# Optimization experiments

Measured on AMD Instinct MI355X. Metric: run time of the kernel, lower is better.

The kernel has to match this reference:

```python
import jax, jax.numpy as jnp
import numpy as np

PROJ_DIM = 128
TEMP = 0.1
CLAMP_VAL = 50.0
EPS = 1e-6


def _coords(H, W):
    # [H*W, 2] grid of (x, y) coordinates, matching torch meshgrid indexing='ij'
    xs = jnp.arange(W, dtype=jnp.float32)
    ys = jnp.arange(H, dtype=jnp.float32)
    grid_y, grid_x = jnp.meshgrid(ys, xs, indexing='ij')
    return jnp.stack([grid_x.reshape(-1), grid_y.reshape(-1)], axis=-1)


def setup_inputs() -> dict:
    key = jax.random.key(0)
    k1, k2 = jax.random.split(key)
    B, C, H, W = 2, 128, 96, 96
    fL = jax.random.normal(k1, (B, C, H, W), dtype=jnp.float32)
    fR = jax.random.normal(k2, (B, C, H, W), dtype=jnp.float32)
    return {"fL": fL, "fR": fR}


def reference(fL, fR):
    B, C, H, W = fL.shape
    HW = H * W
    scale = jnp.float32(np.sqrt(PROJ_DIM))

    # L2-normalize over channel dim with epsilon clamp
    fLn = fL / jnp.maximum(jnp.linalg.norm(fL, axis=1, keepdims=True), EPS)
    fRn = fR / jnp.maximum(jnp.linalg.norm(fR, axis=1, keepdims=True), EPS)

    q = fLn.reshape(B, C, HW).transpose(0, 2, 1).astype(jnp.float32)  # [B, HW, C]
    k = fRn.reshape(B, C, HW).astype(jnp.float32)                      # [B, C, HW]

    coords = _coords(H, W)  # [HW, 2]

    # Global correlation: [B, HW, HW] (chunking in the original is math-equivalent)
    corr = jnp.einsum('bqc,bck->bqk', q, k) / scale
    corr = jnp.clip(corr / TEMP, -CLAMP_VAL, CLAMP_VAL)
    prob = jax.nn.softmax(corr, axis=-1)

    expected_pos = prob @ coords                 # [B, HW, 2]
    max_prob = jnp.max(prob, axis=-1)            # [B, HW]

    flow_abs = expected_pos.reshape(B, H, W, 2).transpose(0, 3, 1, 2)  # [B, 2, H, W]
    conf = max_prob.reshape(B, 1, H, W)

    src = coords.reshape(H, W, 2).transpose(2, 0, 1)[None]  # [1, 2, H, W]
    flow = (flow_abs - src).astype(fL.dtype)
    conf = conf.astype(fL.dtype)
    return flow, conf
```

## Files before the change

kernel.cpp:

```cpp
#include <hip/hip_runtime.h>
#include <stdint.h>

#define HW 9216
#define CDIM 128
#define WIDTH 96
#define BATCH 2

#define QSCALE 1.2753324954171245f

typedef _Float16 half8 __attribute__((ext_vector_type(8)));
typedef float float4v __attribute__((ext_vector_type(4)));
typedef float float2v __attribute__((ext_vector_type(2)));

__global__ __launch_bounds__(256) void norm_kernel(const float* __restrict__ fL,
                                                   const float* __restrict__ fR,
                                                   _Float16* __restrict__ Qh,
                                                   _Float16* __restrict__ Kh)
{
    __shared__ float ssred[4][64];
    __shared__ _Float16 ot[64 * 130];

    const float* src = (blockIdx.y == 0) ? fL : fR;
    _Float16* dst    = (blockIdx.y == 0) ? Qh : Kh;
    const float outScale = (blockIdx.y == 0) ? QSCALE : 1.0f;

    const int t = threadIdx.x;
    const int pos_l = t & 63, cg = t >> 6;
    const int pos0 = blockIdx.x * 64;
    const int b = pos0 / HW, pos_in = pos0 % HW + pos_l;

    const float* p = src + (size_t)b * CDIM * HW + pos_in;

    float v[32];
    float ss = 0.f;
    #pragma unroll
    for (int j = 0; j < 32; ++j) {
        v[j] = p[(size_t)(cg * 32 + j) * HW];
        ss += v[j] * v[j];
    }
    ssred[cg][pos_l] = ss;
    __syncthreads();
    float tot = ssred[0][pos_l] + ssred[1][pos_l] + ssred[2][pos_l] + ssred[3][pos_l];
    float scale = outScale / fmaxf(sqrtf(tot), 1e-6f);

    #pragma unroll
    for (int j = 0; j < 32; ++j)
        ot[pos_l * 130 + cg * 32 + j] = (_Float16)(v[j] * scale);
    __syncthreads();

    uint4* og = (uint4*)(dst + (size_t)(b * HW + pos0 % HW + 0) * CDIM);
    #pragma unroll
    for (int i = 0; i < 4; ++i) {
        int idx = i * 256 + t;
        int row = idx >> 4, chunk = idx & 15;
        og[idx] = *(const uint4*)&ot[row * 130 + chunk * 8];
    }
}

__global__ __launch_bounds__(256) void attn_kernel(const _Float16* __restrict__ Qh,
                                                   const _Float16* __restrict__ Kh,
                                                   float4* __restrict__ part)
{
    __shared__ _Float16 Ks[2 * 64 * 128];

    const int qt = blockIdx.x, split = blockIdx.y, b = blockIdx.z;
    const int t = threadIdx.x;
    const int lane = t & 63, wave = t >> 6;
    const int wq = wave >> 1, wk = wave & 1;
    const int lane15 = lane & 15, quad = lane >> 4;

    half8 af[2][4];
    {
        const char* qb = (const char*)(Qh +
            ((size_t)(b * HW + qt * 64 + wq * 32 + lane15)) * CDIM);
        #pragma unroll
        for (int mt = 0; mt < 2; ++mt)
            #pragma unroll
            for (int kc = 0; kc < 4; ++kc)
                af[mt][kc] = *(const half8*)(qb + mt * 16 * 256 + kc * 64 + quad * 16);
    }

    const int kbase0 = split * 1152;
    const char* kp0 = (const char*)(Kh + (size_t)b * HW * CDIM) + (size_t)kbase0 * 256;

    int voff[4];
    #pragma unroll
    for (int i = 0; i < 4; ++i) {
        int r = wave * 16 + i * 4 + quad;
        voff[i] = r * 256 + ((lane15 ^ (r & 15)) << 4);
    }

    #define STAGE(TILE, BUF)                                                     \
        {                                                                        \
            const char* kb_ = kp0 + (TILE) * 16384;                              \
            _Float16* db_ = &Ks[(BUF) * 8192 + wave * 16 * 128];                 \
            _Pragma("unroll")                                                    \
            for (int i_ = 0; i_ < 4; ++i_)                                       \
                __builtin_amdgcn_global_load_lds(                                \
                    (const __attribute__((address_space(1))) uint32_t*)(kb_ + voff[i_]), \
                    (__attribute__((address_space(3))) uint32_t*)(db_ + i_ * 4 * 128),   \
                    16, 0, 0);                                                   \
        }

    int rdoff[2][4];
    #pragma unroll
    for (int nt = 0; nt < 2; ++nt)
        #pragma unroll
        for (int kc = 0; kc < 4; ++kc)
            rdoff[nt][kc] = ((wk * 32 + nt * 16 + lane15) << 8) +
                            (((kc * 4 + quad) ^ lane15) << 4);
    const char* ksb = (const char*)&Ks[0];

    float xph[3][2], yph[3][2];
    {
        int off0 = wk * 32 + lane15;
        #pragma unroll
        for (int p = 0; p < 3; ++p) {
            #pragma unroll
            for (int nt = 0; nt < 2; ++nt) {
                int k = p * 64 + off0 + nt * 16;
                xph[p][nt] = (float)(k % 96);
                yph[p][nt] = (float)(split * 12 + k / 96);
            }
        }
    }

    float2v l2[4], ax2[4], ay2[4], mx2[4];
    #pragma unroll
    for (int p = 0; p < 4; ++p) {
        l2[p] = (float2v)0.f; ax2[p] = (float2v)0.f; ay2[p] = (float2v)0.f;
        mx2[p] = (float2v)(-1.0e30f);
    }

    STAGE(0, 0);
    __syncthreads();

    #pragma unroll
    for (int kt = 0; kt < 18; ++kt) {
        const int cur = kt & 1;
        const int phase = kt % 3;
        const float yadd = (float)(2 * (kt / 3));

        if (kt < 17) STAGE(kt + 1, 1 - cur);

        float4v acc[2][2];
        #pragma unroll
        for (int kc = 0; kc < 4; ++kc) {
            half8 bf[2];
            #pragma unroll
            for (int nt = 0; nt < 2; ++nt)
                bf[nt] = *(const half8*)(ksb + cur * 16384 + rdoff[nt][kc]);
            #pragma unroll
            for (int mt = 0; mt < 2; ++mt)
                #pragma unroll
                for (int nt = 0; nt < 2; ++nt)
                    acc[mt][nt] = __builtin_amdgcn_mfma_f32_16x16x32_f16(
                        af[mt][kc], bf[nt],
                        (kc == 0) ? (float4v)0.f : acc[mt][nt], 0, 0, 0);
        }

        #pragma unroll
        for (int nt = 0; nt < 2; ++nt) {
            float2v xf2 = (float2v)(xph[phase][nt]);
            float2v yf2 = (float2v)(yph[phase][nt] + yadd);
            #pragma unroll
            for (int mt = 0; mt < 2; ++mt) {
                #pragma unroll
                for (int rp = 0; rp < 2; ++rp) {
                    float2v lg;
                    lg.x = acc[mt][nt][2 * rp];
                    lg.y = acc[mt][nt][2 * rp + 1];
                    float2v e;
                    e.x = __builtin_amdgcn_exp2f(lg.x);
                    e.y = __builtin_amdgcn_exp2f(lg.y);
                    int p = mt * 2 + rp;
                    l2[p]  += e;
                    ax2[p] += e * xf2;
                    ay2[p] += e * yf2;
                    mx2[p] = __builtin_elementwise_max(mx2[p], lg);
                }
            }
        }
        __syncthreads();
    }

    #pragma unroll
    for (int p = 0; p < 4; ++p) {
        #pragma unroll
        for (int m = 1; m < 16; m <<= 1) {
            l2[p].x  += __shfl_xor(l2[p].x,  m, 64);
            l2[p].y  += __shfl_xor(l2[p].y,  m, 64);
            ax2[p].x += __shfl_xor(ax2[p].x, m, 64);
            ax2[p].y += __shfl_xor(ax2[p].y, m, 64);
            ay2[p].x += __shfl_xor(ay2[p].x, m, 64);
            ay2[p].y += __shfl_xor(ay2[p].y, m, 64);
            mx2[p].x  = fmaxf(mx2[p].x, __shfl_xor(mx2[p].x, m, 64));
            mx2[p].y  = fmaxf(mx2[p].y, __shfl_xor(mx2[p].y, m, 64));
        }
    }

    if (lane15 == 0) {
        #pragma unroll
        for (int p = 0; p < 4; ++p) {
            int mt = p >> 1, rp = p & 1;
            #pragma unroll
            for (int comp = 0; comp < 2; ++comp) {
                int r = 2 * rp + comp;
                int row = qt * 64 + wq * 32 + mt * 16 + quad * 4 + r;
                float lv  = comp ? l2[p].y  : l2[p].x;
                float axv = comp ? ax2[p].y : ax2[p].x;
                float ayv = comp ? ay2[p].y : ay2[p].x;
                float mxv = __builtin_amdgcn_exp2f(comp ? mx2[p].y : mx2[p].x);
                part[(size_t)(split * 2 + wk) * (BATCH * HW) + b * HW + row] =
                    make_float4(lv, axv, ayv, mxv);
            }
        }
    }
    #undef STAGE
}

__global__ __launch_bounds__(256) void combine_kernel(const float4* __restrict__ part,
                                                      float* __restrict__ out)
{
    int tid = blockIdx.x * 256 + threadIdx.x;
    int b = tid / HW, pos = tid % HW;
    float l = 0.f, ax = 0.f, ay = 0.f, mx = 0.f;
    #pragma unroll
    for (int s = 0; s < 16; ++s) {
        float4 v = part[(size_t)s * (BATCH * HW) + tid];
        l += v.x; ax += v.y; ay += v.z; mx = fmaxf(mx, v.w);
    }
    float inv = 1.0f / l;
    int x = pos % WIDTH, y = pos / WIDTH;
    out[(size_t)b * 2 * HW + pos]           = ax * inv - (float)x;
    out[(size_t)b * 2 * HW + HW + pos]      = ay * inv - (float)y;
    out[(size_t)BATCH * 2 * HW + (size_t)b * HW + pos] = mx * inv;
}

extern "C" void kernel_launch(void* const* d_in, const int* in_sizes, int n_in,
                              void* d_out, int out_size, void* d_ws, size_t ws_size,
                              hipStream_t stream)
{
    const float* fL = (const float*)d_in[0];
    const float* fR = (const float*)d_in[1];
    float* out = (float*)d_out;

    char* ws = (char*)d_ws;
    const size_t QH_BYTES = (size_t)BATCH * HW * CDIM * sizeof(_Float16);
    _Float16* Qh  = (_Float16*)ws;
    _Float16* Kh  = (_Float16*)(ws + QH_BYTES);
    float4*   part = (float4*)(ws + 2 * QH_BYTES);

    norm_kernel<<<dim3((BATCH * HW) / 64, 2), 256, 0, stream>>>(fL, fR, Qh, Kh);
    attn_kernel<<<dim3(HW / 64, 8, BATCH), 256, 0, stream>>>(Qh, Kh, part);
    combine_kernel<<<dim3((BATCH * HW) / 256), 256, 0, stream>>>(part, out);
}
```

Before: 134.8 us.

## Load K fragments directly from global into registers, dropping LDS staging

Removes the LDS double-buffer for K tiles and the per-tile block barriers. Each wave now loads its own K fragments from global memory straight into registers, prefetching the next tile into a second register set. This drops the shared-memory traffic and synchronisation, but each K row is now fetched by two waves (both wq halves) instead of once per block, and register pressure rises.

```diff
diff --git a/kernel.cpp b/kernel.cpp
--- a/kernel.cpp
+++ b/kernel.cpp
@@ -61,8 +61,6 @@
                                                    const _Float16* __restrict__ Kh,
                                                    float4* __restrict__ part)
 {
-    __shared__ _Float16 Ks[2 * 64 * 128];
-
     const int qt = blockIdx.x, split = blockIdx.y, b = blockIdx.z;
     const int t = threadIdx.x;
     const int lane = t & 63, wave = t >> 6;
@@ -83,33 +81,12 @@
     const int kbase0 = split * 1152;
     const char* kp0 = (const char*)(Kh + (size_t)b * HW * CDIM) + (size_t)kbase0 * 256;
 
-    int voff[4];
-    #pragma unroll
-    for (int i = 0; i < 4; ++i) {
-        int r = wave * 16 + i * 4 + quad;
-        voff[i] = r * 256 + ((lane15 ^ (r & 15)) << 4);
-    }
-
-    #define STAGE(TILE, BUF)                                                     \
-        {                                                                        \
-            const char* kb_ = kp0 + (TILE) * 16384;                              \
-            _Float16* db_ = &Ks[(BUF) * 8192 + wave * 16 * 128];                 \
-            _Pragma("unroll")                                                    \
-            for (int i_ = 0; i_ < 4; ++i_)                                       \
-                __builtin_amdgcn_global_load_lds(                                \
-                    (const __attribute__((address_space(1))) uint32_t*)(kb_ + voff[i_]), \
-                    (__attribute__((address_space(3))) uint32_t*)(db_ + i_ * 4 * 128),   \
-                    16, 0, 0);                                                   \
-        }
-
-    int rdoff[2][4];
+    int kvoff[2][4];
     #pragma unroll
     for (int nt = 0; nt < 2; ++nt)
         #pragma unroll
         for (int kc = 0; kc < 4; ++kc)
-            rdoff[nt][kc] = ((wk * 32 + nt * 16 + lane15) << 8) +
-                            (((kc * 4 + quad) ^ lane15) << 4);
-    const char* ksb = (const char*)&Ks[0];
+            kvoff[nt][kc] = ((wk * 32 + nt * 16 + lane15) << 8) + kc * 64 + quad * 16;
 
     float xph[3][2], yph[3][2];
     {
@@ -132,32 +109,38 @@
         mx2[p] = (float2v)(-1.0e30f);
     }
 
-    STAGE(0, 0);
-    __syncthreads();
+    half8 bf[2][4];
+    #pragma unroll
+    for (int nt = 0; nt < 2; ++nt)
+        #pragma unroll
+        for (int kc = 0; kc < 4; ++kc)
+            bf[nt][kc] = *(const half8*)(kp0 + kvoff[nt][kc]);
 
     #pragma unroll
     for (int kt = 0; kt < 18; ++kt) {
-        const int cur = kt & 1;
         const int phase = kt % 3;
         const float yadd = (float)(2 * (kt / 3));
 
-        if (kt < 17) STAGE(kt + 1, 1 - cur);
+        half8 bfn[2][4];
+        if (kt < 17) {
+            const char* kpn = kp0 + (kt + 1) * 16384;
+            #pragma unroll
+            for (int nt = 0; nt < 2; ++nt)
+                #pragma unroll
+                for (int kc = 0; kc < 4; ++kc)
+                    bfn[nt][kc] = *(const half8*)(kpn + kvoff[nt][kc]);
+        }
 
         float4v acc[2][2];
         #pragma unroll
-        for (int kc = 0; kc < 4; ++kc) {
-            half8 bf[2];
-            #pragma unroll
-            for (int nt = 0; nt < 2; ++nt)
-                bf[nt] = *(const half8*)(ksb + cur * 16384 + rdoff[nt][kc]);
+        for (int kc = 0; kc < 4; ++kc)
             #pragma unroll
             for (int mt = 0; mt < 2; ++mt)
                 #pragma unroll
                 for (int nt = 0; nt < 2; ++nt)
                     acc[mt][nt] = __builtin_amdgcn_mfma_f32_16x16x32_f16(
-                        af[mt][kc], bf[nt],
+                        af[mt][kc], bf[nt][kc],
                         (kc == 0) ? (float4v)0.f : acc[mt][nt], 0, 0, 0);
-        }
 
         #pragma unroll
         for (int nt = 0; nt < 2; ++nt) {
@@ -181,7 +164,14 @@
                 }
             }
         }
-        __syncthreads();
+
+        if (kt < 17) {
+            #pragma unroll
+            for (int nt = 0; nt < 2; ++nt)
+                #pragma unroll
+                for (int kc = 0; kc < 4; ++kc)
+                    bf[nt][kc] = bfn[nt][kc];
+        }
     }
 
     #pragma unroll
@@ -216,7 +206,6 @@
             }
         }
     }
-    #undef STAGE
 }
 
 __global__ __launch_bounds__(256) void combine_kernel(const float4* __restrict__ part,
```

Result: slower. 221.7 us (+64.5%).
